# Kernel tuning notes

Measured on AMD Instinct MI355X. Metric: run time of the kernel, lower is better.

The kernel has to match this reference:

```python
import jax, jax.numpy as jnp
import numpy as np

N = 100_000      # nodes
E = 3_200_000    # edges (avg degree 32)
F_IN = 64        # num_node_features
G = 256          # graphs in batch


def _lin(key, fan_in, fan_out):
    kw, kb = jax.random.split(key)
    bound = 1.0 / np.sqrt(fan_in)
    W = jax.random.uniform(kw, (fan_in, fan_out), jnp.float32, -bound, bound)
    b = jax.random.uniform(kb, (fan_out,), jnp.float32, -bound, bound)
    return W, b


def setup_inputs() -> dict:
    key = jax.random.key(0)
    ks = jax.random.split(key, 9)
    x = jax.random.normal(ks[0], (N, F_IN), jnp.float32)
    edge_index = jax.random.randint(ks[1], (2, E), 0, N, dtype=jnp.int64)
    batch = jnp.sort(jax.random.randint(ks[2], (N,), 0, G, dtype=jnp.int64))
    W1, b1 = _lin(ks[3], F_IN, 60)
    W2, b2 = _lin(ks[4], 60, 50)
    Wf1, bf1 = _lin(ks[5], 50, 30)
    Wf2, bf2 = _lin(ks[6], 30, 20)
    Wf3, bf3 = _lin(ks[7], 20, 10)
    Wo, bo = _lin(ks[8], 10, 1)
    return {"x": x, "edge_index": edge_index, "batch": batch,
            "W1": W1, "b1": b1, "W2": W2, "b2": b2,
            "Wf1": Wf1, "bf1": bf1, "Wf2": Wf2, "bf2": bf2,
            "Wf3": Wf3, "bf3": bf3, "Wo": Wo, "bo": bo}


def _gcn_norm(edge_index, n_nodes):
    # add self loops, then symmetric D^{-1/2} (A+I) D^{-1/2} edge weights
    loop = jnp.arange(n_nodes, dtype=edge_index.dtype)
    src = jnp.concatenate([edge_index[0], loop])
    dst = jnp.concatenate([edge_index[1], loop])
    deg = jax.ops.segment_sum(jnp.ones_like(dst, dtype=jnp.float32), dst,
                              num_segments=n_nodes)
    dinv = jax.lax.rsqrt(deg)  # deg >= 1 thanks to self loops
    norm = dinv[src] * dinv[dst]
    return src, dst, norm


def _gcn_conv(h, W, b, src, dst, norm, n_nodes):
    h = h @ W                                            # [N, out]
    msg = h[src] * norm[:, None]                         # gather over edges
    agg = jax.ops.segment_sum(msg, dst, num_segments=n_nodes)
    return agg + b


def reference(x, edge_index, batch, W1, b1, W2, b2,
              Wf1, bf1, Wf2, bf2, Wf3, bf3, Wo, bo):
    n_nodes = x.shape[0]
    src, dst, norm = _gcn_norm(edge_index, n_nodes)
    h = _gcn_conv(x, W1, b1, src, dst, norm, n_nodes)    # [N, 60]
    h = _gcn_conv(h, W2, b2, src, dst, norm, n_nodes)    # [N, 50]
    # global_add_pool over graph ids
    g = jax.ops.segment_sum(h, batch, num_segments=G)    # [G, 50]
    # MLP stack (no nonlinearities in the original forward)
    g = g @ Wf1 + bf1
    g = g @ Wf2 + bf2
    g = g @ Wf3 + bf3
    return g @ Wo + bo                                   # [G, 1]
```

## Files before the change

### kernel.cpp

```cpp
#include <hip/hip_runtime.h>


#define RSHIFT 7
#define RNODES 128
#define NB_MAX 1024
#define GRID 512
#define THREADS 512
#define STAGE_CAP 8192
#define BCAP 6144

__global__ void collapse_weights_k(
    const float* __restrict__ W1, const float* __restrict__ b1,
    const float* __restrict__ W2, const float* __restrict__ b2,
    const float* __restrict__ Wf1, const float* __restrict__ bf1,
    const float* __restrict__ Wf2, const float* __restrict__ bf2,
    const float* __restrict__ Wf3, const float* __restrict__ bf3,
    const float* __restrict__ Wo, const float* __restrict__ bo,
    float* __restrict__ w1c, float* __restrict__ sc,
    int* __restrict__ cursor, float* __restrict__ out, int G)
{
    __shared__ float wo[10], w3[20], w2[30], w1[50], w2c[60];
    __shared__ float c0s;
    const int t = threadIdx.x;
    for (int b = t; b < NB_MAX; b += 64) cursor[b] = 0;
    if (t < 10) wo[t] = Wo[t];
    __syncthreads();
    if (t < 20) { float s = 0.f; for (int j = 0; j < 10; ++j) s += Wf3[t*10+j]*wo[j]; w3[t] = s; }
    __syncthreads();
    if (t < 30) { float s = 0.f; for (int j = 0; j < 20; ++j) s += Wf2[t*20+j]*w3[j]; w2[t] = s; }
    __syncthreads();
    if (t < 50) { float s = 0.f; for (int j = 0; j < 30; ++j) s += Wf1[t*30+j]*w2[j]; w1[t] = s; }
    __syncthreads();
    if (t < 60) { float s = 0.f; for (int j = 0; j < 50; ++j) s += W2[t*50+j]*w1[j]; w2c[t] = s; }
    __syncthreads();
    { float s = 0.f; for (int j = 0; j < 60; ++j) s += W1[t*60+j]*w2c[j]; w1c[t] = s; }
    if (t == 0) {
        float c1 = 0.f; for (int j = 0; j < 60; ++j) c1 += b1[j]*w2c[j];
        float c2 = 0.f; for (int j = 0; j < 50; ++j) c2 += b2[j]*w1[j];
        float c0 = bo[0];
        for (int j = 0; j < 30; ++j) c0 += bf1[j]*w2[j];
        for (int j = 0; j < 20; ++j) c0 += bf2[j]*w3[j];
        for (int j = 0; j < 10; ++j) c0 += bf3[j]*wo[j];
        sc[0] = c1; sc[1] = c2; sc[2] = c0;
        c0s = c0;
    }
    __syncthreads();
    for (int g = t; g < G; g += 64) out[g] = c0s;
}

__global__ __launch_bounds__(THREADS, 4)
void scatter_u_k(const float* __restrict__ x, const float* __restrict__ w1c,
                 float* __restrict__ u,
                 const int* __restrict__ src, const int* __restrict__ dst,
                 int E, int n, int npb, int chunk, int nb,
                 int* __restrict__ cursor, unsigned int* __restrict__ binned) {
    __shared__ int hist[NB_MAX];
    __shared__ int tbase[NB_MAX];
    __shared__ int adj[NB_MAX];
    __shared__ int sums[THREADS];
    __shared__ unsigned int staged[STAGE_CAP];
    __shared__ unsigned short bof[STAGE_CAP];
    const int tid = threadIdx.x;
    const int bx = blockIdx.x;

    {
        const int grp = tid >> 4, sub = tid & 15;
        float4 wv = *reinterpret_cast<const float4*>(w1c + sub * 4);
        int base = bx * npb;
        for (int p = 0; p * 32 < npb; ++p) {
            int nl = p * 32 + grp;
            int g = base + nl;
            bool ok = (nl < npb) && (g < n);
            float val = 0.f;
            if (ok) {
                float4 xv = *reinterpret_cast<const float4*>(
                    x + (size_t)g * 64 + sub * 4);
                val = xv.x*wv.x + xv.y*wv.y + xv.z*wv.z + xv.w*wv.w;
            }
            val += __shfl_down(val, 8, 16);
            val += __shfl_down(val, 4, 16);
            val += __shfl_down(val, 2, 16);
            val += __shfl_down(val, 1, 16);
            if (ok && sub == 0) u[g] = val;
        }
    }

    hist[tid] = 0; hist[tid + THREADS] = 0;
    __syncthreads();
    int e0 = bx * chunk;
    int e1 = e0 + chunk; if (e1 > E) e1 = E;
    const int QMAX = STAGE_CAP / (THREADS * 4);
    unsigned int pk[QMAX * 4];
    int bk[QMAX * 4];
    int rk[QMAX * 4];
    int nv[QMAX];
    #pragma unroll
    for (int j = 0; j < QMAX; ++j) {
        int i = e0 + tid * 4 + j * (THREADS * 4);
        int cnt = e1 - i; if (cnt > 4) cnt = 4; if (cnt < 0) cnt = 0;
        nv[j] = cnt;
        if (cnt == 4) {
            int4 s4 = *reinterpret_cast<const int4*>(src + i);
            int4 d4 = *reinterpret_cast<const int4*>(dst + i);
            pk[j*4+0] = (unsigned)s4.x | ((unsigned)(d4.x & (RNODES-1)) << 17);
            pk[j*4+1] = (unsigned)s4.y | ((unsigned)(d4.y & (RNODES-1)) << 17);
            pk[j*4+2] = (unsigned)s4.z | ((unsigned)(d4.z & (RNODES-1)) << 17);
            pk[j*4+3] = (unsigned)s4.w | ((unsigned)(d4.w & (RNODES-1)) << 17);
            bk[j*4+0] = d4.x >> RSHIFT; bk[j*4+1] = d4.y >> RSHIFT;
            bk[j*4+2] = d4.z >> RSHIFT; bk[j*4+3] = d4.w >> RSHIFT;
            rk[j*4+0] = atomicAdd(&hist[bk[j*4+0]], 1);
            rk[j*4+1] = atomicAdd(&hist[bk[j*4+1]], 1);
            rk[j*4+2] = atomicAdd(&hist[bk[j*4+2]], 1);
            rk[j*4+3] = atomicAdd(&hist[bk[j*4+3]], 1);
        } else {
            #pragma unroll
            for (int l = 0; l < 4; ++l) {
                if (l < cnt) {
                    int s = src[i + l], d = dst[i + l];
                    pk[j*4+l] = (unsigned)s | ((unsigned)(d & (RNODES-1)) << 17);
                    bk[j*4+l] = d >> RSHIFT;
                    rk[j*4+l] = atomicAdd(&hist[bk[j*4+l]], 1);
                }
            }
        }
    }
    __syncthreads();
    int h0 = hist[2*tid], h1 = hist[2*tid+1];
    int pair = h0 + h1;
    sums[tid] = pair;
    __syncthreads();
    for (int off = 1; off < THREADS; off <<= 1) {
        int a = (tid >= off) ? sums[tid - off] : 0;
        __syncthreads();
        sums[tid] += a;
        __syncthreads();
    }
    int excl = sums[tid] - pair;
    tbase[2*tid] = excl;
    tbase[2*tid+1] = excl + h0;
    {
        int b0 = 2*tid, b1 = 2*tid + 1;
        if (b0 < nb && h0 > 0) {
            int r = atomicAdd(&cursor[b0], h0);
            adj[b0] = b0 * BCAP + r - excl;
        }
        if (b1 < nb && h1 > 0) {
            int r = atomicAdd(&cursor[b1], h1);
            adj[b1] = b1 * BCAP + r - (excl + h0);
        }
    }
    __syncthreads();
    #pragma unroll
    for (int j = 0; j < QMAX; ++j) {
        #pragma unroll
        for (int l = 0; l < 4; ++l) {
            if (l < nv[j]) {
                int b = bk[j*4+l];
                int slot = tbase[b] + rk[j*4+l];
                staged[slot] = pk[j*4+l];
                bof[slot] = (unsigned short)b;
            }
        }
    }
    __syncthreads();
    int tcount = e1 - e0;
    for (int s = tid; s < tcount; s += THREADS) {
        int b = bof[s];
        binned[adj[b] + s] = staged[s];
    }
}

__global__ void degree_dinv_k(const unsigned int* __restrict__ binned,
                              const int* __restrict__ cursor,
                              const float* __restrict__ u,
                              float* __restrict__ dinv, float* __restrict__ w, int n) {
    __shared__ int cnt[RNODES];
    int tid = threadIdx.x, b = blockIdx.x;
    if (tid < RNODES) cnt[tid] = 0;
    __syncthreads();
    int s0 = b * BCAP;
    int c = cursor[b];
    if (c > BCAP) c = BCAP;
    int nvec = c >> 2;
    for (int k = tid; k < nvec; k += blockDim.x) {
        uint4 p = *reinterpret_cast<const uint4*>(binned + s0 + 4 * k);
        atomicAdd(&cnt[p.x >> 17], 1);
        atomicAdd(&cnt[p.y >> 17], 1);
        atomicAdd(&cnt[p.z >> 17], 1);
        atomicAdd(&cnt[p.w >> 17], 1);
    }
    int i = 4 * nvec + tid;
    if (i < c) atomicAdd(&cnt[binned[s0 + i] >> 17], 1);
    __syncthreads();
    int g = (b << RSHIFT) + tid;
    if (tid < RNODES && g < n) {
        float d = rsqrtf((float)(cnt[tid] + 1));
        dinv[g] = d;
        w[g] = d * u[g];
    }
}

__global__ void conv_mid_k(const unsigned int* __restrict__ binned,
                           const int* __restrict__ cursor,
                           const float* __restrict__ w, const float* __restrict__ dinv,
                           const float* __restrict__ u, const float* __restrict__ sc,
                           float* __restrict__ v, float* __restrict__ wb, int n) {
    __shared__ float acc[RNODES];
    int tid = threadIdx.x, b = blockIdx.x;
    if (tid < RNODES) acc[tid] = 0.f;
    __syncthreads();
    int s0 = b * BCAP;
    int cnt = cursor[b];
    if (cnt > BCAP) cnt = BCAP;
    int nvec = cnt >> 2;
    for (int k = tid; k < nvec; k += blockDim.x) {
        uint4 p = *reinterpret_cast<const uint4*>(binned + s0 + 4 * k);
        float wx = w[p.x & 0x1FFFF];
        float wy = w[p.y & 0x1FFFF];
        float wz = w[p.z & 0x1FFFF];
        float ww = w[p.w & 0x1FFFF];
        atomicAdd(&acc[p.x >> 17], wx);
        atomicAdd(&acc[p.y >> 17], wy);
        atomicAdd(&acc[p.z >> 17], wz);
        atomicAdd(&acc[p.w >> 17], ww);
    }
    int i = 4 * nvec + tid;
    if (i < cnt) { unsigned p = binned[s0 + i]; atomicAdd(&acc[p >> 17], w[p & 0x1FFFF]); }
    __syncthreads();
    int g = (b << RSHIFT) + tid;
    if (tid < RNODES && g < n) {
        float di = dinv[g];
        float val = sc[0] + di * acc[tid] + di * di * u[g];
        v[g] = val;
        wb[g] = di * val;
    }
}

__global__ void conv_final_k(const unsigned int* __restrict__ binned,
                             const int* __restrict__ cursor,
                             const float* __restrict__ wb, const float* __restrict__ dinv,
                             const float* __restrict__ v, const float* __restrict__ sc,
                             const int* __restrict__ batch, float* __restrict__ out, int n) {
    __shared__ float acc[RNODES];
    __shared__ float tbuf[RNODES];
    __shared__ int gbuf[RNODES];
    int tid = threadIdx.x, b = blockIdx.x;
    if (tid < RNODES) acc[tid] = 0.f;
    __syncthreads();
    int s0 = b * BCAP;
    int cnt = cursor[b];
    if (cnt > BCAP) cnt = BCAP;
    int nvec = cnt >> 2;
    for (int k = tid; k < nvec; k += blockDim.x) {
        uint4 p = *reinterpret_cast<const uint4*>(binned + s0 + 4 * k);
        float wx = wb[p.x & 0x1FFFF];
        float wy = wb[p.y & 0x1FFFF];
        float wz = wb[p.z & 0x1FFFF];
        float ww = wb[p.w & 0x1FFFF];
        atomicAdd(&acc[p.x >> 17], wx);
        atomicAdd(&acc[p.y >> 17], wy);
        atomicAdd(&acc[p.z >> 17], wz);
        atomicAdd(&acc[p.w >> 17], ww);
    }
    int i = 4 * nvec + tid;
    if (i < cnt) { unsigned p = binned[s0 + i]; atomicAdd(&acc[p >> 17], wb[p & 0x1FFFF]); }
    __syncthreads();
    int g = (b << RSHIFT) + tid;
    float tval = 0.f; int gid = -1;
    if (tid < RNODES && g < n) {
        float di = dinv[g];
        tval = sc[1] + di * acc[tid] + di * di * v[g];
        gid = batch[g];
    }
    if (tid < RNODES) { tbuf[tid] = tval; gbuf[tid] = gid; }
    __syncthreads();
    if (tid < RNODES && g < n) {
        bool head = (tid == 0) || (gbuf[tid - 1] != gid);
        if (head) {
            float s = 0.f;
            int i2 = tid;
            while (i2 < RNODES && gbuf[i2] == gid) { s += tbuf[i2]; ++i2; }
            atomicAdd(&out[gid], s);
        }
    }
}

extern "C" void kernel_launch(void* const* d_in, const int* in_sizes, int n_in,
                              void* d_out, int out_size, void* d_ws, size_t ws_size,
                              hipStream_t stream)
{
    const float* x    = (const float*)d_in[0];
    const int*   ei   = (const int*)d_in[1];
    const int*   batch= (const int*)d_in[2];
    const float* W1   = (const float*)d_in[3];
    const float* b1   = (const float*)d_in[4];
    const float* W2   = (const float*)d_in[5];
    const float* b2   = (const float*)d_in[6];
    const float* Wf1  = (const float*)d_in[7];
    const float* bf1  = (const float*)d_in[8];
    const float* Wf2  = (const float*)d_in[9];
    const float* bf2  = (const float*)d_in[10];
    const float* Wf3  = (const float*)d_in[11];
    const float* bf3  = (const float*)d_in[12];
    const float* Wo   = (const float*)d_in[13];
    const float* bo   = (const float*)d_in[14];
    float* out = (float*)d_out;

    const int n = in_sizes[0] / 64;
    const int E = in_sizes[1] / 2;
    const int G = out_size;
    const int* src = ei;
    const int* dst = ei + E;
    const int nb = (n + RNODES - 1) >> RSHIFT;

    float* ws_f = (float*)d_ws;
    int*   ws_i = (int*)d_ws;
    float* w1c    = ws_f;
    float* sc     = ws_f + 64;
    int*   cursor = ws_i + 128;
    size_t off_u  = 128 + (size_t)NB_MAX;
    float* u      = ws_f + off_u;
    float* dinv   = u + n;
    float* w      = dinv + n;
    float* v      = w + n;
    float* wb     = v + n;
    size_t off_b  = off_u + 5*(size_t)n;
    off_b = (off_b + 3) & ~(size_t)3;
    unsigned int* binned = (unsigned int*)(ws_f + off_b);

    int chunk = (E + GRID - 1) / GRID;
    chunk = (chunk + 3) & ~3;
    int npb = (n + GRID - 1) / GRID;

    hipLaunchKernelGGL(collapse_weights_k, dim3(1), dim3(64), 0, stream,
                       W1, b1, W2, b2, Wf1, bf1, Wf2, bf2, Wf3, bf3, Wo, bo,
                       w1c, sc, cursor, out, G);
    hipLaunchKernelGGL(scatter_u_k, dim3(GRID), dim3(THREADS), 0, stream,
                       x, w1c, u, src, dst, E, n, npb, chunk, nb, cursor, binned);
    hipLaunchKernelGGL(degree_dinv_k, dim3(nb), dim3(512), 0, stream,
                       binned, cursor, u, dinv, w, n);
    hipLaunchKernelGGL(conv_mid_k, dim3(nb), dim3(512), 0, stream,
                       binned, cursor, w, dinv, u, sc, v, wb, n);
    hipLaunchKernelGGL(conv_final_k, dim3(nb), dim3(512), 0, stream,
                       binned, cursor, wb, dinv, v, sc, batch, out, n);
}
```

Measured before the change: 203.1 us.

## Use 512-node destination buckets and fixed 4096-edge scatter tiles

Widens each destination bucket from 128 to 512 nodes, so there are about 196 buckets. Each conv kernel block now has 1024 threads and keeps a larger shared accumulator. The scatter pass becomes fixed 4096-edge tiles, one per block, with 8 edges per thread held in registers, a 256-entry scan and byte-sized bucket tags. The aim is fewer, larger contiguous runs when writing edges into bins and less scan and staging overhead. The cost is that the conv kernels run with fewer blocks than the GPU has compute units, which may leave the machine under-used.

```diff
diff --git a/kernel.cpp b/kernel.cpp
--- a/kernel.cpp
+++ b/kernel.cpp
@@ -1,13 +1,13 @@
 #include <hip/hip_runtime.h>
 
 
-#define RSHIFT 7
-#define RNODES 128
-#define NB_MAX 1024
-#define GRID 512
-#define THREADS 512
-#define STAGE_CAP 8192
-#define BCAP 6144
+#define RSHIFT 9
+#define RNODES 512
+#define NB_MAX 256
+#define STHREADS 512
+#define CTHREADS 1024
+#define STAGE_CAP 4096
+#define BCAP 20480
 
 __global__ void collapse_weights_k(
     const float* __restrict__ W1, const float* __restrict__ b1,
@@ -48,18 +48,18 @@
     for (int g = t; g < G; g += 64) out[g] = c0s;
 }
 
-__global__ __launch_bounds__(THREADS, 4)
+__global__ __launch_bounds__(STHREADS, 4)
 void scatter_u_k(const float* __restrict__ x, const float* __restrict__ w1c,
                  float* __restrict__ u,
                  const int* __restrict__ src, const int* __restrict__ dst,
-                 int E, int n, int npb, int chunk, int nb,
+                 int E, int n, int npb, int nb,
                  int* __restrict__ cursor, unsigned int* __restrict__ binned) {
     __shared__ int hist[NB_MAX];
     __shared__ int tbase[NB_MAX];
     __shared__ int adj[NB_MAX];
-    __shared__ int sums[THREADS];
+    __shared__ int sums[NB_MAX];
     __shared__ unsigned int staged[STAGE_CAP];
-    __shared__ unsigned short bof[STAGE_CAP];
+    __shared__ unsigned char bof[STAGE_CAP];
     const int tid = threadIdx.x;
     const int bx = blockIdx.x;
 
@@ -85,88 +85,90 @@
         }
     }
 
-    hist[tid] = 0; hist[tid + THREADS] = 0;
-    __syncthreads();
-    int e0 = bx * chunk;
-    int e1 = e0 + chunk; if (e1 > E) e1 = E;
-    const int QMAX = STAGE_CAP / (THREADS * 4);
-    unsigned int pk[QMAX * 4];
-    int bk[QMAX * 4];
-    int rk[QMAX * 4];
-    int nv[QMAX];
-    #pragma unroll
-    for (int j = 0; j < QMAX; ++j) {
-        int i = e0 + tid * 4 + j * (THREADS * 4);
-        int cnt = e1 - i; if (cnt > 4) cnt = 4; if (cnt < 0) cnt = 0;
-        nv[j] = cnt;
-        if (cnt == 4) {
-            int4 s4 = *reinterpret_cast<const int4*>(src + i);
-            int4 d4 = *reinterpret_cast<const int4*>(dst + i);
-            pk[j*4+0] = (unsigned)s4.x | ((unsigned)(d4.x & (RNODES-1)) << 17);
-            pk[j*4+1] = (unsigned)s4.y | ((unsigned)(d4.y & (RNODES-1)) << 17);
-            pk[j*4+2] = (unsigned)s4.z | ((unsigned)(d4.z & (RNODES-1)) << 17);
-            pk[j*4+3] = (unsigned)s4.w | ((unsigned)(d4.w & (RNODES-1)) << 17);
-            bk[j*4+0] = d4.x >> RSHIFT; bk[j*4+1] = d4.y >> RSHIFT;
-            bk[j*4+2] = d4.z >> RSHIFT; bk[j*4+3] = d4.w >> RSHIFT;
-            rk[j*4+0] = atomicAdd(&hist[bk[j*4+0]], 1);
-            rk[j*4+1] = atomicAdd(&hist[bk[j*4+1]], 1);
-            rk[j*4+2] = atomicAdd(&hist[bk[j*4+2]], 1);
-            rk[j*4+3] = atomicAdd(&hist[bk[j*4+3]], 1);
-        } else {
-            #pragma unroll
-            for (int l = 0; l < 4; ++l) {
-                if (l < cnt) {
-                    int s = src[i + l], d = dst[i + l];
-                    pk[j*4+l] = (unsigned)s | ((unsigned)(d & (RNODES-1)) << 17);
-                    bk[j*4+l] = d >> RSHIFT;
-                    rk[j*4+l] = atomicAdd(&hist[bk[j*4+l]], 1);
-                }
-            }
+    if (tid < NB_MAX) hist[tid] = 0;
+    __syncthreads();
+    int e0 = bx * STAGE_CAP;
+    int e1 = e0 + STAGE_CAP; if (e1 > E) e1 = E;
+
+    unsigned pk0=0,pk1=0,pk2=0,pk3=0,pk4=0,pk5=0,pk6=0,pk7=0;
+    int bk0=0,bk1=0,bk2=0,bk3=0,bk4=0,bk5=0,bk6=0,bk7=0;
+    int rk0=0,rk1=0,rk2=0,rk3=0,rk4=0,rk5=0,rk6=0,rk7=0;
+    int iA = e0 + tid * 4;
+    int iB = iA + STHREADS * 4;
+    int cA = e1 - iA; if (cA > 4) cA = 4; if (cA < 0) cA = 0;
+    int cB = e1 - iB; if (cB > 4) cB = 4; if (cB < 0) cB = 0;
+
+    if (cA == 4) {
+        int4 s4 = *reinterpret_cast<const int4*>(src + iA);
+        int4 d4 = *reinterpret_cast<const int4*>(dst + iA);
+        pk0 = (unsigned)s4.x | ((unsigned)(d4.x & (RNODES-1)) << 17);
+        pk1 = (unsigned)s4.y | ((unsigned)(d4.y & (RNODES-1)) << 17);
+        pk2 = (unsigned)s4.z | ((unsigned)(d4.z & (RNODES-1)) << 17);
+        pk3 = (unsigned)s4.w | ((unsigned)(d4.w & (RNODES-1)) << 17);
+        bk0 = d4.x >> RSHIFT; bk1 = d4.y >> RSHIFT;
+        bk2 = d4.z >> RSHIFT; bk3 = d4.w >> RSHIFT;
+        rk0 = atomicAdd(&hist[bk0], 1);
+        rk1 = atomicAdd(&hist[bk1], 1);
+        rk2 = atomicAdd(&hist[bk2], 1);
+        rk3 = atomicAdd(&hist[bk3], 1);
+    } else {
+        if (cA > 0) { int s=src[iA],   d=dst[iA];   pk0=(unsigned)s|((unsigned)(d&(RNODES-1))<<17); bk0=d>>RSHIFT; rk0=atomicAdd(&hist[bk0],1); }
+        if (cA > 1) { int s=src[iA+1], d=dst[iA+1]; pk1=(unsigned)s|((unsigned)(d&(RNODES-1))<<17); bk1=d>>RSHIFT; rk1=atomicAdd(&hist[bk1],1); }
+        if (cA > 2) { int s=src[iA+2], d=dst[iA+2]; pk2=(unsigned)s|((unsigned)(d&(RNODES-1))<<17); bk2=d>>RSHIFT; rk2=atomicAdd(&hist[bk2],1); }
+    }
+    if (cB == 4) {
+        int4 s4 = *reinterpret_cast<const int4*>(src + iB);
+        int4 d4 = *reinterpret_cast<const int4*>(dst + iB);
+        pk4 = (unsigned)s4.x | ((unsigned)(d4.x & (RNODES-1)) << 17);
+        pk5 = (unsigned)s4.y | ((unsigned)(d4.y & (RNODES-1)) << 17);
+        pk6 = (unsigned)s4.z | ((unsigned)(d4.z & (RNODES-1)) << 17);
+        pk7 = (unsigned)s4.w | ((unsigned)(d4.w & (RNODES-1)) << 17);
+        bk4 = d4.x >> RSHIFT; bk5 = d4.y >> RSHIFT;
+        bk6 = d4.z >> RSHIFT; bk7 = d4.w >> RSHIFT;
+        rk4 = atomicAdd(&hist[bk4], 1);
+        rk5 = atomicAdd(&hist[bk5], 1);
+        rk6 = atomicAdd(&hist[bk6], 1);
+        rk7 = atomicAdd(&hist[bk7], 1);
+    } else {
+        if (cB > 0) { int s=src[iB],   d=dst[iB];   pk4=(unsigned)s|((unsigned)(d&(RNODES-1))<<17); bk4=d>>RSHIFT; rk4=atomicAdd(&hist[bk4],1); }
+        if (cB > 1) { int s=src[iB+1], d=dst[iB+1]; pk5=(unsigned)s|((unsigned)(d&(RNODES-1))<<17); bk5=d>>RSHIFT; rk5=atomicAdd(&hist[bk5],1); }
+        if (cB > 2) { int s=src[iB+2], d=dst[iB+2]; pk6=(unsigned)s|((unsigned)(d&(RNODES-1))<<17); bk6=d>>RSHIFT; rk6=atomicAdd(&hist[bk6],1); }
+    }
+    __syncthreads();
+
+    int h = (tid < NB_MAX) ? hist[tid] : 0;
+    if (tid < NB_MAX) sums[tid] = h;
+    __syncthreads();
+    for (int off = 1; off < NB_MAX; off <<= 1) {
+        int a = (tid >= off && tid < NB_MAX) ? sums[tid - off] : 0;
+        __syncthreads();
+        if (tid < NB_MAX) sums[tid] += a;
+        __syncthreads();
+    }
+    if (tid < NB_MAX) {
+        int excl = sums[tid] - h;
+        tbase[tid] = excl;
+        if (tid < nb && h > 0) {
+            int r = atomicAdd(&cursor[tid], h);
+            adj[tid] = tid * BCAP + r - excl;
         }
     }
     __syncthreads();
-    int h0 = hist[2*tid], h1 = hist[2*tid+1];
-    int pair = h0 + h1;
-    sums[tid] = pair;
-    __syncthreads();
-    for (int off = 1; off < THREADS; off <<= 1) {
-        int a = (tid >= off) ? sums[tid - off] : 0;
-        __syncthreads();
-        sums[tid] += a;
-        __syncthreads();
-    }
-    int excl = sums[tid] - pair;
-    tbase[2*tid] = excl;
-    tbase[2*tid+1] = excl + h0;
-    {
-        int b0 = 2*tid, b1 = 2*tid + 1;
-        if (b0 < nb && h0 > 0) {
-            int r = atomicAdd(&cursor[b0], h0);
-            adj[b0] = b0 * BCAP + r - excl;
-        }
-        if (b1 < nb && h1 > 0) {
-            int r = atomicAdd(&cursor[b1], h1);
-            adj[b1] = b1 * BCAP + r - (excl + h0);
-        }
-    }
-    __syncthreads();
-    #pragma unroll
-    for (int j = 0; j < QMAX; ++j) {
-        #pragma unroll
-        for (int l = 0; l < 4; ++l) {
-            if (l < nv[j]) {
-                int b = bk[j*4+l];
-                int slot = tbase[b] + rk[j*4+l];
-                staged[slot] = pk[j*4+l];
-                bof[slot] = (unsigned short)b;
-            }
-        }
-    }
-    __syncthreads();
+
+    if (cA > 0) { int s2 = tbase[bk0] + rk0; staged[s2] = pk0; bof[s2] = (unsigned char)bk0; }
+    if (cA > 1) { int s2 = tbase[bk1] + rk1; staged[s2] = pk1; bof[s2] = (unsigned char)bk1; }
+    if (cA > 2) { int s2 = tbase[bk2] + rk2; staged[s2] = pk2; bof[s2] = (unsigned char)bk2; }
+    if (cA > 3) { int s2 = tbase[bk3] + rk3; staged[s2] = pk3; bof[s2] = (unsigned char)bk3; }
+    if (cB > 0) { int s2 = tbase[bk4] + rk4; staged[s2] = pk4; bof[s2] = (unsigned char)bk4; }
+    if (cB > 1) { int s2 = tbase[bk5] + rk5; staged[s2] = pk5; bof[s2] = (unsigned char)bk5; }
+    if (cB > 2) { int s2 = tbase[bk6] + rk6; staged[s2] = pk6; bof[s2] = (unsigned char)bk6; }
+    if (cB > 3) { int s2 = tbase[bk7] + rk7; staged[s2] = pk7; bof[s2] = (unsigned char)bk7; }
+    __syncthreads();
+
     int tcount = e1 - e0;
-    for (int s = tid; s < tcount; s += THREADS) {
-        int b = bof[s];
-        binned[adj[b] + s] = staged[s];
+    for (int s2 = tid; s2 < tcount; s2 += STHREADS) {
+        int b = bof[s2];
+        binned[adj[b] + s2] = staged[s2];
     }
 }
 
@@ -178,7 +180,7 @@
     int tid = threadIdx.x, b = blockIdx.x;
     if (tid < RNODES) cnt[tid] = 0;
     __syncthreads();
-    int s0 = b * BCAP;
+    size_t s0 = (size_t)b * BCAP;
     int c = cursor[b];
     if (c > BCAP) c = BCAP;
     int nvec = c >> 2;
@@ -209,7 +211,7 @@
     int tid = threadIdx.x, b = blockIdx.x;
     if (tid < RNODES) acc[tid] = 0.f;
     __syncthreads();
-    int s0 = b * BCAP;
+    size_t s0 = (size_t)b * BCAP;
     int cnt = cursor[b];
     if (cnt > BCAP) cnt = BCAP;
     int nvec = cnt >> 2;
@@ -247,7 +249,7 @@
     int tid = threadIdx.x, b = blockIdx.x;
     if (tid < RNODES) acc[tid] = 0.f;
     __syncthreads();
-    int s0 = b * BCAP;
+    size_t s0 = (size_t)b * BCAP;
     int cnt = cursor[b];
     if (cnt > BCAP) cnt = BCAP;
     int nvec = cnt >> 2;
@@ -328,19 +330,18 @@
     off_b = (off_b + 3) & ~(size_t)3;
     unsigned int* binned = (unsigned int*)(ws_f + off_b);
 
-    int chunk = (E + GRID - 1) / GRID;
-    chunk = (chunk + 3) & ~3;
-    int npb = (n + GRID - 1) / GRID;
+    const int NT = (E + STAGE_CAP - 1) / STAGE_CAP;
+    const int npb = (n + NT - 1) / NT;
 
     hipLaunchKernelGGL(collapse_weights_k, dim3(1), dim3(64), 0, stream,
                        W1, b1, W2, b2, Wf1, bf1, Wf2, bf2, Wf3, bf3, Wo, bo,
                        w1c, sc, cursor, out, G);
-    hipLaunchKernelGGL(scatter_u_k, dim3(GRID), dim3(THREADS), 0, stream,
-                       x, w1c, u, src, dst, E, n, npb, chunk, nb, cursor, binned);
-    hipLaunchKernelGGL(degree_dinv_k, dim3(nb), dim3(512), 0, stream,
+    hipLaunchKernelGGL(scatter_u_k, dim3(NT), dim3(STHREADS), 0, stream,
+                       x, w1c, u, src, dst, E, n, npb, nb, cursor, binned);
+    hipLaunchKernelGGL(degree_dinv_k, dim3(nb), dim3(CTHREADS), 0, stream,
                        binned, cursor, u, dinv, w, n);
-    hipLaunchKernelGGL(conv_mid_k, dim3(nb), dim3(512), 0, stream,
+    hipLaunchKernelGGL(conv_mid_k, dim3(nb), dim3(CTHREADS), 0, stream,
                        binned, cursor, w, dinv, u, sc, v, wb, n);
-    hipLaunchKernelGGL(conv_final_k, dim3(nb), dim3(512), 0, stream,
+    hipLaunchKernelGGL(conv_final_k, dim3(nb), dim3(CTHREADS), 0, stream,
                        binned, cursor, wb, dinv, v, sc, batch, out, n);
 }
```

Measured after the change: 223.2 us. 1.1x slower.
